# Performance work log

Hardware: AMD Instinct MI355X
Metric: run time of the kernel (lower is better)

## Reference

```python
import jax, jax.numpy as jnp
import numpy as np
import math

N = 20000      # nodes
E = 640000     # edges (avg degree 32)
G = 128        # g_dim (input features)
H1 = 128       # rgcn output dim
H2 = 128       # transformer output dim
R = 8          # num_relations


def setup_inputs() -> dict:
    key = jax.random.key(0)
    ks = jax.random.split(key, 12)
    x = jax.random.normal(ks[0], (N, G), dtype=jnp.float32)
    edge_index = jax.random.randint(ks[1], (2, E), 0, N)
    edge_type = jax.random.randint(ks[2], (E,), 0, R)
    s_in = 1.0 / math.sqrt(G)
    s_h1 = 1.0 / math.sqrt(H1)
    return {
        'x': x,
        'edge_index': edge_index,
        'edge_type': edge_type,
        # RGCNConv params (per-relation weights + root weight + bias)
        'rgcn_weight': jax.random.normal(ks[3], (R, G, H1), dtype=jnp.float32) * s_in,
        'rgcn_root': jax.random.normal(ks[4], (G, H1), dtype=jnp.float32) * s_in,
        'rgcn_bias': jnp.zeros((H1,), dtype=jnp.float32),
        # TransformerConv params (heads=1): query/key/value + skip linear
        'Wq': jax.random.normal(ks[5], (H1, H2), dtype=jnp.float32) * s_h1,
        'bq': jnp.zeros((H2,), dtype=jnp.float32),
        'Wk': jax.random.normal(ks[6], (H1, H2), dtype=jnp.float32) * s_h1,
        'bk': jnp.zeros((H2,), dtype=jnp.float32),
        'Wv': jax.random.normal(ks[7], (H1, H2), dtype=jnp.float32) * s_h1,
        'bv': jnp.zeros((H2,), dtype=jnp.float32),
        'Ws': jax.random.normal(ks[8], (H1, H2), dtype=jnp.float32) * s_h1,
        'bs': jnp.zeros((H2,), dtype=jnp.float32),
    }


def reference(x, edge_index, edge_type, rgcn_weight, rgcn_root, rgcn_bias,
              Wq, bq, Wk, bk, Wv, bv, Ws, bs):
    n = x.shape[0]
    src, dst = edge_index[0], edge_index[1]

    # ---- RGCNConv (aggr='mean' per relation, root weight + bias) ----
    # transform nodes by every relation, then gather per-edge message
    xr = jnp.einsum('ni,rio->nro', x, rgcn_weight)          # [N, R, H1]
    msg = xr[src, edge_type]                                # [E, H1]
    # per (dst, relation) edge counts for mean aggregation
    cnt = jnp.zeros((n, rgcn_weight.shape[0]), x.dtype).at[dst, edge_type].add(1.0)
    denom = jnp.maximum(cnt[dst, edge_type], 1.0)[:, None]  # [E, 1]
    agg = jnp.zeros((n, rgcn_weight.shape[2]), x.dtype).at[dst].add(msg / denom)
    h = agg + x @ rgcn_root + rgcn_bias
    h = jax.nn.relu(h)

    # ---- TransformerConv (heads=1, concat, root_weight=True) ----
    d = Wq.shape[1]
    q = h @ Wq + bq                                          # [N, H2]
    k = h @ Wk + bk
    v = h @ Wv + bv
    score = jnp.sum(q[dst] * k[src], axis=-1) / math.sqrt(d) # [E]
    # softmax over incoming edges of each destination node
    smax = jax.ops.segment_max(score, dst, num_segments=n)   # [N]
    e = jnp.exp(score - smax[dst])                           # [E]
    den = jax.ops.segment_sum(e, dst, num_segments=n)        # [N]
    alpha = e / jnp.maximum(den[dst], 1e-16)                 # [E]
    out = jax.ops.segment_sum(alpha[:, None] * v[src], dst, num_segments=n)
    out = out + h @ Ws + bs                                  # skip connection
    return jax.nn.relu(out)
```

## Files before the change

### kernel.cpp

```cpp
#include <hip/hip_runtime.h>

typedef unsigned short u16;
typedef unsigned int u32;
typedef __attribute__((ext_vector_type(8))) short short8;
typedef __attribute__((ext_vector_type(4))) float f32x4;

#define NN 20000
#define EE 640000
#define SCAN_BLOCKS 80

__device__ inline u16 f2bf(float f) {
    u32 x = __float_as_uint(f);
    return (u16)((x + 0x7FFFu + ((x >> 16) & 1u)) >> 16);
}
__device__ inline float lo16(u32 w) { return __uint_as_float(w << 16); }
__device__ inline float hi16(u32 w) { return __uint_as_float(w & 0xFFFF0000u); }
__device__ inline u32 packbf(float a, float b) { return ((u32)f2bf(b) << 16) | (u32)f2bf(a); }

#define CT_N (EE / 8)
#define CX_N (NN * 32)
#define WP_N (128 * 1152 + 4 * 128 * 128 + 512)
__global__ __launch_bounds__(256) void prep_count(const int* __restrict__ ei,
                                                  const int* __restrict__ et,
                                                  int* __restrict__ cnt, int* __restrict__ rank,
                                                  const float* __restrict__ x,
                                                  const float* rw, const float* root,
                                                  const float* Wq, const float* Wk,
                                                  const float* Wv, const float* Ws,
                                                  const float* bq, const float* bk,
                                                  const float* bv, const float* bs,
                                                  u16* __restrict__ xb,
                                                  u16* wt1, u16* wt2, float* bcat) {
    int idx = blockIdx.x * 256 + threadIdx.x;
    if (idx < CT_N) {
#pragma unroll
        for (int j = 0; j < 8; j++) {
            int e = idx + j * CT_N;
            int dst = ei[EE + e];
            int r = et[e];
            rank[e] = atomicAdd(&cnt[dst * 8 + r], 1);
        }
        return;
    }
    idx -= CT_N;
    if (idx < CX_N) {
        float4 v = *(const float4*)(x + (size_t)idx * 4);
        uint2 o;
        o.x = packbf(v.x, v.y);
        o.y = packbf(v.z, v.w);
        *(uint2*)(xb + (size_t)idx * 4) = o;
        return;
    }
    idx -= CX_N;
    const int S1 = 128 * 1152, S2 = 4 * 128 * 128;
    if (idx < S1) {
        int o = idx / 1152, k = idx - o * 1152;
        float v = (k < 1024) ? rw[k * 128 + o] : root[(k - 1024) * 128 + o];
        wt1[idx] = f2bf(v);
    } else if (idx < S1 + S2) {
        int j = idx - S1;
        int y = j >> 14, rem = j & 16383, o = rem >> 7, i = rem & 127;
        const float* W = (y == 0) ? Wq : (y == 1) ? Wk : (y == 2) ? Wv : Ws;
        wt2[j] = f2bf(W[i * 128 + o]);
    } else if (idx < S1 + S2 + 512) {
        int j = idx - (S1 + S2);
        int y = j >> 7, c = j & 127;
        const float* b = (y == 0) ? bq : (y == 1) ? bk : (y == 2) ? bv : bs;
        bcat[j] = b[c];
    }
}

__global__ __launch_bounds__(256) void scan_phase1(const int* __restrict__ cnt,
                                                   int* __restrict__ deg_pref,
                                                   int* __restrict__ blk_sums) {
    __shared__ int lds[256];
    int t = threadIdx.x;
    int n = blockIdx.x * 256 + t;
    int d = 0;
    if (n < NN) {
        int4 c0 = *(const int4*)(cnt + n * 8);
        int4 c1 = *(const int4*)(cnt + n * 8 + 4);
        d = c0.x + c0.y + c0.z + c0.w + c1.x + c1.y + c1.z + c1.w;
    }
    lds[t] = d;
    __syncthreads();
    for (int o = 1; o < 256; o <<= 1) {
        int v = (t >= o) ? lds[t - o] : 0;
        __syncthreads();
        lds[t] += v;
        __syncthreads();
    }
    if (n < NN) deg_pref[n] = lds[t];
    if (t == 255) blk_sums[blockIdx.x] = lds[255];
}

__global__ __launch_bounds__(256) void scan_phase3(const int* __restrict__ cnt,
                                                   const int* __restrict__ deg_pref,
                                                   const int* __restrict__ blk_sums,
                                                   int* __restrict__ row_off,
                                                   int* __restrict__ srt) {
    __shared__ int bs_lds[128];
    int t = threadIdx.x;
    if (t < 128) {
        int v = (t < SCAN_BLOCKS) ? blk_sums[t] : 0;
        bs_lds[t] = v;
    }
    __syncthreads();
    if (t < 128) {
        for (int o = 1; o < 128; o <<= 1) {
            int a = (t >= o) ? bs_lds[t - o] : 0;
            __syncthreads();
            bs_lds[t] += a;
            __syncthreads();
        }
    } else {
        for (int o = 1; o < 128; o <<= 1) {
            __syncthreads();
            __syncthreads();
        }
    }
    int blk_excl = (blockIdx.x > 0) ? bs_lds[blockIdx.x - 1] : 0;
    int n = blockIdx.x * 256 + t;
    if (n >= NN) return;
    int4 c0 = *(const int4*)(cnt + n * 8);
    int4 c1 = *(const int4*)(cnt + n * 8 + 4);
    int deg = c0.x + c0.y + c0.z + c0.w + c1.x + c1.y + c1.z + c1.w;
    int start = blk_excl + deg_pref[n] - deg;
    row_off[n] = start;
    int sub = start;
    int o[8];
    o[0] = sub; sub += c0.x;
    o[1] = sub; sub += c0.y;
    o[2] = sub; sub += c0.z;
    o[3] = sub; sub += c0.w;
    o[4] = sub; sub += c1.x;
    o[5] = sub; sub += c1.y;
    o[6] = sub; sub += c1.z;
    o[7] = sub; sub += c1.w;
    *(int4*)(srt + n * 8) = make_int4(o[0], o[1], o[2], o[3]);
    *(int4*)(srt + n * 8 + 4) = make_int4(o[4], o[5], o[6], o[7]);
    if (n == NN - 1) row_off[NN] = sub;
}

__global__ void scatter_kernel(const int* __restrict__ ei, const int* __restrict__ et,
                               const int* __restrict__ srt, const int* __restrict__ rank,
                               int* __restrict__ es) {
    int base = blockIdx.x * 2048 + threadIdx.x;
#pragma unroll
    for (int j = 0; j < 8; j++) {
        int e = base + j * 256;
        if (e < EE) {
            int dst = ei[EE + e];
            int src = ei[e];
            int r = et[e];
            es[srt[dst * 8 + r] + rank[e]] = src;
        }
    }
}

__global__ __launch_bounds__(256) void gemm_rgcn_fused(const u16* __restrict__ xb,
                                                       const int* __restrict__ srt,
                                                       const int* __restrict__ cnt,
                                                       const int* __restrict__ es,
                                                       const u16* __restrict__ Bt1,
                                                       const float* __restrict__ bias1,
                                                       const u16* __restrict__ Wt2,
                                                       const float* __restrict__ bcat,
                                                       u16* __restrict__ Cq, u16* __restrict__ Ckv,
                                                       u16* __restrict__ Cs) {
    __shared__ u16 As[16 * 136];
    __shared__ u16 Bs[128 * 136];
    int tid = threadIdx.x;
    int w = tid >> 6;
    int lane = tid & 63;
    int quad = lane >> 4;
    int ml = lane & 15;
    int nq = w;
    int block_m = blockIdx.x * 16;

    int rbase = tid >> 4;
    int cb = (tid & 15) * 8;

    int node_l = tid >> 4;
    int th = tid & 15;
    int db = th * 8;
    int gnode = block_m + node_l;

    f32x4 acc[2];
#pragma unroll
    for (int i = 0; i < 2; i++) acc[i] = (f32x4){0.f, 0.f, 0.f, 0.f};

#pragma unroll 1
    for (int slot = 0; slot < 8; slot++) {
        int kb = slot * 128;
#pragma unroll
        for (int rep = 0; rep < 8; rep++) {
            int r = rbase + rep * 16;
            short8 val = *(const short8*)(Bt1 + (long)r * 1152 + kb + cb);
            *(short8*)(Bs + r * 136 + cb) = val;
        }
        int c = cnt[gnode * 8 + slot];
        int p0 = srt[gnode * 8 + slot];
        float a0 = 0.f, a1 = 0.f, a2 = 0.f, a3 = 0.f, a4 = 0.f, a5 = 0.f, a6 = 0.f, a7 = 0.f;
        int i = 0;
        for (; i + 2 <= c; i += 2) {
            int s0 = es[p0 + i], s1 = es[p0 + i + 1];
            uint4 wa = *(const uint4*)(xb + (long)s0 * 128 + db);
            uint4 wb = *(const uint4*)(xb + (long)s1 * 128 + db);
            a0 += lo16(wa.x) + lo16(wb.x);
            a1 += hi16(wa.x) + hi16(wb.x);
            a2 += lo16(wa.y) + lo16(wb.y);
            a3 += hi16(wa.y) + hi16(wb.y);
            a4 += lo16(wa.z) + lo16(wb.z);
            a5 += hi16(wa.z) + hi16(wb.z);
            a6 += lo16(wa.w) + lo16(wb.w);
            a7 += hi16(wa.w) + hi16(wb.w);
        }
        if (i < c) {
            int s0 = es[p0 + i];
            uint4 wa = *(const uint4*)(xb + (long)s0 * 128 + db);
            a0 += lo16(wa.x); a1 += hi16(wa.x); a2 += lo16(wa.y); a3 += hi16(wa.y);
            a4 += lo16(wa.z); a5 += hi16(wa.z); a6 += lo16(wa.w); a7 += hi16(wa.w);
        }
        float inv = 1.0f / (float)(c > 1 ? c : 1);
        uint4 o0 = make_uint4(packbf(a0 * inv, a1 * inv), packbf(a2 * inv, a3 * inv),
                              packbf(a4 * inv, a5 * inv), packbf(a6 * inv, a7 * inv));
        *(uint4*)(As + node_l * 136 + db) = o0;
        __syncthreads();
#pragma unroll
        for (int ks = 0; ks < 4; ks++) {
            short8 af = *(const short8*)(As + ml * 136 + ks * 32 + quad * 8);
#pragma unroll
            for (int nt = 0; nt < 2; nt++) {
                short8 bfr = *(const short8*)(Bs + (nq * 32 + nt * 16 + ml) * 136 + ks * 32 + quad * 8);
                acc[nt] = __builtin_amdgcn_mfma_f32_16x16x32_bf16(af, bfr, acc[nt], 0, 0, 0);
            }
        }
        __syncthreads();
    }
    {
#pragma unroll
        for (int rep = 0; rep < 8; rep++) {
            int r = rbase + rep * 16;
            short8 val = *(const short8*)(Bt1 + (long)r * 1152 + 1024 + cb);
            *(short8*)(Bs + r * 136 + cb) = val;
        }
        short8 val = *(const short8*)(xb + (long)(block_m + rbase) * 128 + cb);
        *(short8*)(As + rbase * 136 + cb) = val;
        __syncthreads();
#pragma unroll
        for (int ks = 0; ks < 4; ks++) {
            short8 af = *(const short8*)(As + ml * 136 + ks * 32 + quad * 8);
#pragma unroll
            for (int nt = 0; nt < 2; nt++) {
                short8 bfr = *(const short8*)(Bs + (nq * 32 + nt * 16 + ml) * 136 + ks * 32 + quad * 8);
                acc[nt] = __builtin_amdgcn_mfma_f32_16x16x32_bf16(af, bfr, acc[nt], 0, 0, 0);
            }
        }
        __syncthreads();
    }
#pragma unroll
    for (int nt = 0; nt < 2; nt++) {
        int col = nq * 32 + nt * 16 + ml;
        float bv = bias1[col];
#pragma unroll
        for (int i = 0; i < 4; i++) {
            int r = quad * 4 + i;
            As[r * 136 + col] = f2bf(fmaxf(acc[nt][i] + bv, 0.f));
        }
    }
    __syncthreads();

#pragma unroll 1
    for (int y = 0; y < 4; y++) {
#pragma unroll
        for (int rep = 0; rep < 8; rep++) {
            int r = rbase + rep * 16;
            short8 val = *(const short8*)(Wt2 + (long)y * 16384 + (long)r * 128 + cb);
            *(short8*)(Bs + r * 136 + cb) = val;
        }
        __syncthreads();
        f32x4 acc2[2];
#pragma unroll
        for (int i = 0; i < 2; i++) acc2[i] = (f32x4){0.f, 0.f, 0.f, 0.f};
#pragma unroll
        for (int ks = 0; ks < 4; ks++) {
            short8 af = *(const short8*)(As + ml * 136 + ks * 32 + quad * 8);
#pragma unroll
            for (int nt = 0; nt < 2; nt++) {
                short8 bfr = *(const short8*)(Bs + (nq * 32 + nt * 16 + ml) * 136 + ks * 32 + quad * 8);
                acc2[nt] = __builtin_amdgcn_mfma_f32_16x16x32_bf16(af, bfr, acc2[nt], 0, 0, 0);
            }
        }
        u16* C;
        int ldc;
        if (y == 0) { C = Cq; ldc = 128; }
        else if (y == 1) { C = Ckv; ldc = 256; }
        else if (y == 2) { C = Ckv + 128; ldc = 256; }
        else { C = Cs; ldc = 128; }
#pragma unroll
        for (int nt = 0; nt < 2; nt++) {
            int col = nq * 32 + nt * 16 + ml;
            float bv = bcat[y * 128 + col];
#pragma unroll
            for (int i = 0; i < 4; i++) {
                int gr = block_m + quad * 4 + i;
                C[(long)gr * ldc + col] = f2bf(acc2[nt][i] + bv);
            }
        }
        __syncthreads();
    }
}

__global__ __launch_bounds__(128) void attn_kernel(const u16* __restrict__ q,
                                                   const u16* __restrict__ kv,
                                                   const u16* __restrict__ skip,
                                                   const int* __restrict__ row_off,
                                                   const int* __restrict__ es,
                                                   float* __restrict__ out) {
    int node = blockIdx.x * 8 + (threadIdx.x >> 4);
    int lane = threadIdx.x & 15;
    if (node >= NN) return;
    int p0 = row_off[node], p1 = row_off[node + 1];
    uint4 qw = *(const uint4*)(q + (long)node * 128 + lane * 8);
    float q0 = lo16(qw.x), q1 = hi16(qw.x), q2 = lo16(qw.y), q3 = hi16(qw.y);
    float q4 = lo16(qw.z), q5 = hi16(qw.z), q6 = lo16(qw.w), q7 = hi16(qw.w);
    const float SC = 0.08838834764831845f;
    float l = 0.f;
    float a0 = 0.f, a1 = 0.f, a2 = 0.f, a3 = 0.f, a4 = 0.f, a5 = 0.f, a6 = 0.f, a7 = 0.f;
    int p = p0;
    for (; p + 4 <= p1; p += 4) {
        const u16* b0 = kv + (long)es[p] * 256 + lane * 8;
        const u16* b1 = kv + (long)es[p + 1] * 256 + lane * 8;
        const u16* b2 = kv + (long)es[p + 2] * 256 + lane * 8;
        const u16* b3 = kv + (long)es[p + 3] * 256 + lane * 8;
        uint4 k0 = *(const uint4*)b0;
        uint4 k1 = *(const uint4*)b1;
        uint4 k2 = *(const uint4*)b2;
        uint4 k3 = *(const uint4*)b3;
        uint4 v0 = *(const uint4*)(b0 + 128);
        uint4 v1 = *(const uint4*)(b1 + 128);
        uint4 v2 = *(const uint4*)(b2 + 128);
        uint4 v3 = *(const uint4*)(b3 + 128);
        float t0 = q0 * lo16(k0.x) + q1 * hi16(k0.x) + q2 * lo16(k0.y) + q3 * hi16(k0.y) +
                   q4 * lo16(k0.z) + q5 * hi16(k0.z) + q6 * lo16(k0.w) + q7 * hi16(k0.w);
        float t1 = q0 * lo16(k1.x) + q1 * hi16(k1.x) + q2 * lo16(k1.y) + q3 * hi16(k1.y) +
                   q4 * lo16(k1.z) + q5 * hi16(k1.z) + q6 * lo16(k1.w) + q7 * hi16(k1.w);
        float t2 = q0 * lo16(k2.x) + q1 * hi16(k2.x) + q2 * lo16(k2.y) + q3 * hi16(k2.y) +
                   q4 * lo16(k2.z) + q5 * hi16(k2.z) + q6 * lo16(k2.w) + q7 * hi16(k2.w);
        float t3 = q0 * lo16(k3.x) + q1 * hi16(k3.x) + q2 * lo16(k3.y) + q3 * hi16(k3.y) +
                   q4 * lo16(k3.z) + q5 * hi16(k3.z) + q6 * lo16(k3.w) + q7 * hi16(k3.w);
#pragma unroll
        for (int off = 8; off >= 1; off >>= 1) {
            t0 += __shfl_xor(t0, off, 16);
            t1 += __shfl_xor(t1, off, 16);
            t2 += __shfl_xor(t2, off, 16);
            t3 += __shfl_xor(t3, off, 16);
        }
        float w0 = __expf(fminf(t0 * SC, 70.f));
        float w1 = __expf(fminf(t1 * SC, 70.f));
        float w2 = __expf(fminf(t2 * SC, 70.f));
        float w3 = __expf(fminf(t3 * SC, 70.f));
        l += (w0 + w1) + (w2 + w3);
        a0 += w0 * lo16(v0.x) + w1 * lo16(v1.x) + w2 * lo16(v2.x) + w3 * lo16(v3.x);
        a1 += w0 * hi16(v0.x) + w1 * hi16(v1.x) + w2 * hi16(v2.x) + w3 * hi16(v3.x);
        a2 += w0 * lo16(v0.y) + w1 * lo16(v1.y) + w2 * lo16(v2.y) + w3 * lo16(v3.y);
        a3 += w0 * hi16(v0.y) + w1 * hi16(v1.y) + w2 * hi16(v2.y) + w3 * hi16(v3.y);
        a4 += w0 * lo16(v0.z) + w1 * lo16(v1.z) + w2 * lo16(v2.z) + w3 * lo16(v3.z);
        a5 += w0 * hi16(v0.z) + w1 * hi16(v1.z) + w2 * hi16(v2.z) + w3 * hi16(v3.z);
        a6 += w0 * lo16(v0.w) + w1 * lo16(v1.w) + w2 * lo16(v2.w) + w3 * lo16(v3.w);
        a7 += w0 * hi16(v0.w) + w1 * hi16(v1.w) + w2 * hi16(v2.w) + w3 * hi16(v3.w);
    }
    for (; p < p1; p++) {
        const u16* b = kv + (long)es[p] * 256 + lane * 8;
        uint4 kw = *(const uint4*)b;
        uint4 vw = *(const uint4*)(b + 128);
        float t = q0 * lo16(kw.x) + q1 * hi16(kw.x) + q2 * lo16(kw.y) + q3 * hi16(kw.y) +
                  q4 * lo16(kw.z) + q5 * hi16(kw.z) + q6 * lo16(kw.w) + q7 * hi16(kw.w);
#pragma unroll
        for (int off = 8; off >= 1; off >>= 1) t += __shfl_xor(t, off, 16);
        float w = __expf(fminf(t * SC, 70.f));
        l += w;
        a0 += w * lo16(vw.x);
        a1 += w * hi16(vw.x);
        a2 += w * lo16(vw.y);
        a3 += w * hi16(vw.y);
        a4 += w * lo16(vw.z);
        a5 += w * hi16(vw.z);
        a6 += w * lo16(vw.w);
        a7 += w * hi16(vw.w);
    }
    float invl = (l > 0.f) ? 1.0f / l : 0.f;
    uint4 sw = *(const uint4*)(skip + (long)node * 128 + lane * 8);
    float4 oa, ob;
    oa.x = fmaxf(a0 * invl + lo16(sw.x), 0.f);
    oa.y = fmaxf(a1 * invl + hi16(sw.x), 0.f);
    oa.z = fmaxf(a2 * invl + lo16(sw.y), 0.f);
    oa.w = fmaxf(a3 * invl + hi16(sw.y), 0.f);
    ob.x = fmaxf(a4 * invl + lo16(sw.z), 0.f);
    ob.y = fmaxf(a5 * invl + hi16(sw.z), 0.f);
    ob.z = fmaxf(a6 * invl + lo16(sw.w), 0.f);
    ob.w = fmaxf(a7 * invl + hi16(sw.w), 0.f);
    *(float4*)(out + (long)node * 128 + lane * 8) = oa;
    *(float4*)(out + (long)node * 128 + lane * 8 + 4) = ob;
}

extern "C" void kernel_launch(void* const* d_in, const int* in_sizes, int n_in,
                              void* d_out, int out_size, void* d_ws, size_t ws_size,
                              hipStream_t stream) {
    const float* x = (const float*)d_in[0];
    const int* ei = (const int*)d_in[1];
    const int* et = (const int*)d_in[2];
    const float* rw = (const float*)d_in[3];
    const float* root = (const float*)d_in[4];
    const float* rbias = (const float*)d_in[5];
    const float* Wq = (const float*)d_in[6];
    const float* bq = (const float*)d_in[7];
    const float* Wk = (const float*)d_in[8];
    const float* bk = (const float*)d_in[9];
    const float* Wv = (const float*)d_in[10];
    const float* bv = (const float*)d_in[11];
    const float* Ws = (const float*)d_in[12];
    const float* bs = (const float*)d_in[13];

    char* ws = (char*)d_ws;
    size_t off = 0;
    auto alloc = [&](size_t b) {
        size_t o = off;
        off = (off + b + 255) & ~(size_t)255;
        return o;
    };
    u16* qv = (u16*)(ws + alloc((size_t)NN * 128 * 2));
    u16* kv = (u16*)(ws + alloc((size_t)NN * 256 * 2));
    u16* skip = (u16*)(ws + alloc((size_t)NN * 128 * 2));
    u16* xb = (u16*)(ws + alloc((size_t)NN * 128 * 2));
    u16* wt1 = (u16*)(ws + alloc((size_t)128 * 1152 * 2));
    u16* wt2 = (u16*)(ws + alloc((size_t)4 * 128 * 128 * 2));
    float* bcat = (float*)(ws + alloc((size_t)512 * 4));
    int* cnt = (int*)(ws + alloc((size_t)NN * 8 * 4));
    int* row_off = (int*)(ws + alloc((size_t)(NN + 1) * 4));
    int* srt = (int*)(ws + alloc((size_t)NN * 8 * 4));
    int* deg_pref = (int*)(ws + alloc((size_t)NN * 4));
    int* blk_sums = (int*)(ws + alloc((size_t)128 * 4));
    int* rank = (int*)(ws + alloc((size_t)EE * 4));
    int* es = (int*)(ws + alloc((size_t)EE * 4));
    (void)ws_size;
    (void)in_sizes;
    (void)n_in;
    (void)out_size;

    hipMemsetAsync(cnt, 0, (size_t)NN * 8 * 4, stream);

    prep_count<<<(CT_N + CX_N + WP_N + 255) / 256, 256, 0, stream>>>(
        ei, et, cnt, rank, x, rw, root, Wq, Wk, Wv, Ws, bq, bk, bv, bs,
        xb, wt1, wt2, bcat);

    scan_phase1<<<SCAN_BLOCKS, 256, 0, stream>>>(cnt, deg_pref, blk_sums);
    scan_phase3<<<SCAN_BLOCKS, 256, 0, stream>>>(cnt, deg_pref, blk_sums, row_off, srt);
    scatter_kernel<<<(EE + 2047) / 2048, 256, 0, stream>>>(ei, et, srt, rank, es);

    gemm_rgcn_fused<<<NN / 16, 256, 0, stream>>>(xb, srt, cnt, es, wt1, rbias, wt2, bcat,
                                                 qv, kv, skip);

    attn_kernel<<<(NN + 7) / 8, 128, 0, stream>>>(qv, kv, skip, row_off, es, (float*)d_out);
}
```

Before: 249.5 us.

## Load MFMA weight fragments directly into registers and double-buffer the A tile

The fused RGCN+projection kernel no longer stages the 128x128 weight tiles through a large shared-memory buffer. Each wave now loads its B fragments straight from global memory into registers. The A tile is double-buffered, which removes one barrier per slot and folds the root-weight slot into the main loop. This cuts LDS use sharply, which may allow higher occupancy, and removes the cooperative copy and its barriers. In exchange it uses more registers and makes global reads of the weights that are less coalesced.

```diff
diff --git a/kernel.cpp b/kernel.cpp
--- a/kernel.cpp
+++ b/kernel.cpp
@@ -168,8 +168,7 @@
                                                        const float* __restrict__ bcat,
                                                        u16* __restrict__ Cq, u16* __restrict__ Ckv,
                                                        u16* __restrict__ Cs) {
-    __shared__ u16 As[16 * 136];
-    __shared__ u16 Bs[128 * 136];
+    __shared__ u16 As[2][16 * 136];
     int tid = threadIdx.x;
     int w = tid >> 6;
     int lane = tid & 63;
@@ -178,87 +177,70 @@
     int nq = w;
     int block_m = blockIdx.x * 16;
 
-    int rbase = tid >> 4;
-    int cb = (tid & 15) * 8;
-
     int node_l = tid >> 4;
     int th = tid & 15;
     int db = th * 8;
     int gnode = block_m + node_l;
 
+    const u16* bp0 = Bt1 + (long)(nq * 32 + ml) * 1152 + quad * 8;
+
     f32x4 acc[2];
 #pragma unroll
     for (int i = 0; i < 2; i++) acc[i] = (f32x4){0.f, 0.f, 0.f, 0.f};
 
 #pragma unroll 1
-    for (int slot = 0; slot < 8; slot++) {
-        int kb = slot * 128;
-#pragma unroll
-        for (int rep = 0; rep < 8; rep++) {
-            int r = rbase + rep * 16;
-            short8 val = *(const short8*)(Bt1 + (long)r * 1152 + kb + cb);
-            *(short8*)(Bs + r * 136 + cb) = val;
-        }
-        int c = cnt[gnode * 8 + slot];
-        int p0 = srt[gnode * 8 + slot];
-        float a0 = 0.f, a1 = 0.f, a2 = 0.f, a3 = 0.f, a4 = 0.f, a5 = 0.f, a6 = 0.f, a7 = 0.f;
-        int i = 0;
-        for (; i + 2 <= c; i += 2) {
-            int s0 = es[p0 + i], s1 = es[p0 + i + 1];
-            uint4 wa = *(const uint4*)(xb + (long)s0 * 128 + db);
-            uint4 wb = *(const uint4*)(xb + (long)s1 * 128 + db);
-            a0 += lo16(wa.x) + lo16(wb.x);
-            a1 += hi16(wa.x) + hi16(wb.x);
-            a2 += lo16(wa.y) + lo16(wb.y);
-            a3 += hi16(wa.y) + hi16(wb.y);
-            a4 += lo16(wa.z) + lo16(wb.z);
-            a5 += hi16(wa.z) + hi16(wb.z);
-            a6 += lo16(wa.w) + lo16(wb.w);
-            a7 += hi16(wa.w) + hi16(wb.w);
-        }
-        if (i < c) {
-            int s0 = es[p0 + i];
-            uint4 wa = *(const uint4*)(xb + (long)s0 * 128 + db);
-            a0 += lo16(wa.x); a1 += hi16(wa.x); a2 += lo16(wa.y); a3 += hi16(wa.y);
-            a4 += lo16(wa.z); a5 += hi16(wa.z); a6 += lo16(wa.w); a7 += hi16(wa.w);
-        }
-        float inv = 1.0f / (float)(c > 1 ? c : 1);
-        uint4 o0 = make_uint4(packbf(a0 * inv, a1 * inv), packbf(a2 * inv, a3 * inv),
-                              packbf(a4 * inv, a5 * inv), packbf(a6 * inv, a7 * inv));
-        *(uint4*)(As + node_l * 136 + db) = o0;
+    for (int slot = 0; slot < 9; slot++) {
+        short8 bf[4][2];
+#pragma unroll
+        for (int ks = 0; ks < 4; ks++)
+#pragma unroll
+            for (int nt = 0; nt < 2; nt++)
+                bf[ks][nt] = *(const short8*)(bp0 + (long)nt * 16 * 1152 + slot * 128 + ks * 32);
+
+        u16* dst = &As[slot & 1][node_l * 136 + db];
+        if (slot < 8) {
+            int c = cnt[gnode * 8 + slot];
+            int p0 = srt[gnode * 8 + slot];
+            float a0 = 0.f, a1 = 0.f, a2 = 0.f, a3 = 0.f, a4 = 0.f, a5 = 0.f, a6 = 0.f, a7 = 0.f;
+            int i = 0;
+            for (; i + 2 <= c; i += 2) {
+                int s0 = es[p0 + i], s1 = es[p0 + i + 1];
+                uint4 wa = *(const uint4*)(xb + (long)s0 * 128 + db);
+                uint4 wb = *(const uint4*)(xb + (long)s1 * 128 + db);
+                a0 += lo16(wa.x) + lo16(wb.x);
+                a1 += hi16(wa.x) + hi16(wb.x);
+                a2 += lo16(wa.y) + lo16(wb.y);
+                a3 += hi16(wa.y) + hi16(wb.y);
+                a4 += lo16(wa.z) + lo16(wb.z);
+                a5 += hi16(wa.z) + hi16(wb.z);
+                a6 += lo16(wa.w) + lo16(wb.w);
+                a7 += hi16(wa.w) + hi16(wb.w);
+            }
+            if (i < c) {
+                int s0 = es[p0 + i];
+                uint4 wa = *(const uint4*)(xb + (long)s0 * 128 + db);
+                a0 += lo16(wa.x); a1 += hi16(wa.x); a2 += lo16(wa.y); a3 += hi16(wa.y);
+                a4 += lo16(wa.z); a5 += hi16(wa.z); a6 += lo16(wa.w); a7 += hi16(wa.w);
+            }
+            float inv = 1.0f / (float)(c > 1 ? c : 1);
+            uint4 o0 = make_uint4(packbf(a0 * inv, a1 * inv), packbf(a2 * inv, a3 * inv),
+                                  packbf(a4 * inv, a5 * inv), packbf(a6 * inv, a7 * inv));
+            *(uint4*)dst = o0;
+        } else {
+            short8 val = *(const short8*)(xb + (long)gnode * 128 + db);
+            *(short8*)dst = val;
+        }
         __syncthreads();
+        const u16* ab = &As[slot & 1][0];
 #pragma unroll
         for (int ks = 0; ks < 4; ks++) {
-            short8 af = *(const short8*)(As + ml * 136 + ks * 32 + quad * 8);
-#pragma unroll
-            for (int nt = 0; nt < 2; nt++) {
-                short8 bfr = *(const short8*)(Bs + (nq * 32 + nt * 16 + ml) * 136 + ks * 32 + quad * 8);
-                acc[nt] = __builtin_amdgcn_mfma_f32_16x16x32_bf16(af, bfr, acc[nt], 0, 0, 0);
-            }
-        }
-        __syncthreads();
-    }
-    {
-#pragma unroll
-        for (int rep = 0; rep < 8; rep++) {
-            int r = rbase + rep * 16;
-            short8 val = *(const short8*)(Bt1 + (long)r * 1152 + 1024 + cb);
-            *(short8*)(Bs + r * 136 + cb) = val;
-        }
-        short8 val = *(const short8*)(xb + (long)(block_m + rbase) * 128 + cb);
-        *(short8*)(As + rbase * 136 + cb) = val;
-        __syncthreads();
-#pragma unroll
-        for (int ks = 0; ks < 4; ks++) {
-            short8 af = *(const short8*)(As + ml * 136 + ks * 32 + quad * 8);
-#pragma unroll
-            for (int nt = 0; nt < 2; nt++) {
-                short8 bfr = *(const short8*)(Bs + (nq * 32 + nt * 16 + ml) * 136 + ks * 32 + quad * 8);
-                acc[nt] = __builtin_amdgcn_mfma_f32_16x16x32_bf16(af, bfr, acc[nt], 0, 0, 0);
-            }
-        }
-        __syncthreads();
-    }
+            short8 af = *(const short8*)(ab + ml * 136 + ks * 32 + quad * 8);
+            acc[0] = __builtin_amdgcn_mfma_f32_16x16x32_bf16(af, bf[ks][0], acc[0], 0, 0, 0);
+            acc[1] = __builtin_amdgcn_mfma_f32_16x16x32_bf16(af, bf[ks][1], acc[1], 0, 0, 0);
+        }
+    }
+    __syncthreads();
+
 #pragma unroll
     for (int nt = 0; nt < 2; nt++) {
         int col = nq * 32 + nt * 16 + ml;
@@ -266,31 +248,28 @@
 #pragma unroll
         for (int i = 0; i < 4; i++) {
             int r = quad * 4 + i;
-            As[r * 136 + col] = f2bf(fmaxf(acc[nt][i] + bv, 0.f));
+            As[0][r * 136 + col] = f2bf(fmaxf(acc[nt][i] + bv, 0.f));
         }
     }
     __syncthreads();
 
 #pragma unroll 1
     for (int y = 0; y < 4; y++) {
-#pragma unroll
-        for (int rep = 0; rep < 8; rep++) {
-            int r = rbase + rep * 16;
-            short8 val = *(const short8*)(Wt2 + (long)y * 16384 + (long)r * 128 + cb);
-            *(short8*)(Bs + r * 136 + cb) = val;
-        }
-        __syncthreads();
+        const u16* wp = Wt2 + (long)y * 16384 + (long)(nq * 32 + ml) * 128 + quad * 8;
+        short8 bf2[4][2];
+#pragma unroll
+        for (int ks = 0; ks < 4; ks++)
+#pragma unroll
+            for (int nt = 0; nt < 2; nt++)
+                bf2[ks][nt] = *(const short8*)(wp + (long)nt * 16 * 128 + ks * 32);
         f32x4 acc2[2];
 #pragma unroll
         for (int i = 0; i < 2; i++) acc2[i] = (f32x4){0.f, 0.f, 0.f, 0.f};
 #pragma unroll
         for (int ks = 0; ks < 4; ks++) {
-            short8 af = *(const short8*)(As + ml * 136 + ks * 32 + quad * 8);
-#pragma unroll
-            for (int nt = 0; nt < 2; nt++) {
-                short8 bfr = *(const short8*)(Bs + (nq * 32 + nt * 16 + ml) * 136 + ks * 32 + quad * 8);
-                acc2[nt] = __builtin_amdgcn_mfma_f32_16x16x32_bf16(af, bfr, acc2[nt], 0, 0, 0);
-            }
+            short8 af = *(const short8*)(&As[0][ml * 136 + ks * 32 + quad * 8]);
+            acc2[0] = __builtin_amdgcn_mfma_f32_16x16x32_bf16(af, bf2[ks][0], acc2[0], 0, 0, 0);
+            acc2[1] = __builtin_amdgcn_mfma_f32_16x16x32_bf16(af, bf2[ks][1], acc2[1], 0, 0, 0);
         }
         u16* C;
         int ldc;
@@ -308,7 +287,6 @@
                 C[(long)gr * ldc + col] = f2bf(acc2[nt][i] + bv);
             }
         }
-        __syncthreads();
     }
 }
 
```

Result: slower. 260.6 us (+4.4%).
